# Performance work log

Measured on AMD Instinct MI355X. Metric: run time of the kernel, lower is better.

## Reference

```python
import jax, jax.numpy as jnp
import numpy as np


def setup_inputs() -> dict:
    key = jax.random.key(0)
    k1, k2 = jax.random.split(key)
    x = jax.random.normal(k1, (16, 64, 224, 224), dtype=jnp.float32)
    # conv weight [out=1, in=2, kh=7, kw=7]; init roughly mimics small-normal init
    conv_w = jax.random.normal(k2, (1, 2, 7, 7), dtype=jnp.float32) * 0.01
    conv_b = jnp.zeros((1,), dtype=jnp.float32)
    return {"x": x, "conv_w": conv_w, "conv_b": conv_b}


def reference(x, conv_w, conv_b):
    # channel-wise mean and max -> [B, 2, H, W]
    avg_out = jnp.mean(x, axis=1, keepdims=True)
    max_out = jnp.max(x, axis=1, keepdims=True)
    feat = jnp.concatenate([avg_out, max_out], axis=1)
    # 2->1 channel 7x7 conv, padding 3 (same)
    y = jax.lax.conv_general_dilated(
        feat, conv_w,
        window_strides=(1, 1),
        padding=((3, 3), (3, 3)),
        dimension_numbers=("NCHW", "OIHW", "NCHW"),
    ) + conv_b[None, :, None, None]
    # sigmoid gate broadcast-multiplied back onto x
    return jax.nn.sigmoid(y) * x
```

## Files before the change

kernel.cpp:

```cpp
#include <hip/hip_runtime.h>
#include <math.h>

#define BB 16
#define CC 64
#define HH 224
#define WW 224
#define HWSZ (HH * WW)
#define HW4 (HWSZ / 4)
#define W4 (WW / 4)
#define R 7
#define TILES (HH / R)
#define FR (R + 6)
#define FW 240
#define T 512
#define NBLK (BB * TILES)

#define TA 256
#define NPIX (BB * HW4)
#define NBLKA (NPIX / TA)

typedef float f32x4 __attribute__((ext_vector_type(4)));

__global__ __launch_bounds__(TA) void reduce_kernel(const float* __restrict__ x,
                                                    float* __restrict__ feat) {
    const int idx = blockIdx.x * TA + threadIdx.x;
    const int b   = idx / HW4;
    const int p   = idx - b * HW4;
    const f32x4* xp = reinterpret_cast<const f32x4*>(x) + (size_t)b * (CC * HW4) + p;

    f32x4 s = {0.f, 0.f, 0.f, 0.f};
    f32x4 m = {-INFINITY, -INFINITY, -INFINITY, -INFINITY};
#pragma unroll 16
    for (int c = 0; c < CC; ++c) {
        f32x4 u = xp[(size_t)c * HW4];
        s += u;
        m[0] = fmaxf(m[0], u[0]); m[1] = fmaxf(m[1], u[1]);
        m[2] = fmaxf(m[2], u[2]); m[3] = fmaxf(m[3], u[3]);
    }
    const float inv = 1.0f / 64.0f;
    f32x4* fav = reinterpret_cast<f32x4*>(feat);
    f32x4* fmx = fav + NPIX;
    fav[idx] = s * inv;
    fmx[idx] = m;
}

__global__ __launch_bounds__(T, 4) void gate_kernel(const float* __restrict__ x,
                                                    const float* __restrict__ feat,
                                                    const float* __restrict__ cw,
                                                    const float* __restrict__ cb,
                                                    float* __restrict__ out) {
    __shared__ float fa[FR * FW];
    __shared__ float fm[FR * FW];
    __shared__ alignas(16) float gate[R * WW];
    __shared__ float wt[98];

    const int blk0 = blockIdx.x;
    const int blk  = (blk0 & 7) * (NBLK / 8) + (blk0 >> 3);
    const int b    = blk >> 5;
    const int tb   = blk & 31;
    const int h0   = tb * R;
    const int t    = threadIdx.x;

    for (int i = t; i < FR * FW; i += T) { fa[i] = 0.f; fm[i] = 0.f; }
    if (t < 98) wt[t] = cw[t];
    __syncthreads();

    const f32x4* fav = reinterpret_cast<const f32x4*>(feat) + (size_t)b * HW4;
    const f32x4* fmx = fav + NPIX;
    for (int q = t; q < 2 * FR * W4; q += T) {
        int plane = (q >= FR * W4);
        int p  = plane ? q - FR * W4 : q;
        int pr = p / W4;
        int pc = p - pr * W4;
        int gh = h0 - 3 + pr;
        if ((unsigned)gh >= (unsigned)HH) continue;
        f32x4 u = (plane ? fmx : fav)[gh * W4 + pc];
        float* dst = (plane ? fm : fa) + pr * FW + 3 + pc * 4;
        dst[0] = u[0]; dst[1] = u[1]; dst[2] = u[2]; dst[3] = u[3];
    }
    __syncthreads();

    const float bias = cb[0];
    for (int p = t; p < R * WW; p += T) {
        int r = p / WW;
        int w = p - r * WW;
        float acc = bias;
#pragma unroll
        for (int kh = 0; kh < 7; ++kh) {
            int ro = (r + kh) * FW + w;
#pragma unroll
            for (int kw = 0; kw < 7; ++kw) {
                acc = fmaf(fa[ro + kw], wt[kh * 7 + kw], acc);
                acc = fmaf(fm[ro + kw], wt[49 + kh * 7 + kw], acc);
            }
        }
        gate[p] = 1.0f / (1.0f + expf(-acc));
    }
    __syncthreads();

    const f32x4* xb = reinterpret_cast<const f32x4*>(x) + (size_t)b * (CC * HW4);
    f32x4* ob = reinterpret_cast<f32x4*>(out) + (size_t)b * (CC * HW4);
    const f32x4* g4 = reinterpret_cast<const f32x4*>(gate);
    const int NP = R * W4;
    for (int i = t; i < CC * NP; i += T) {
        int c  = i / NP;
        int p  = i - c * NP;
        int pr = p / W4;
        int pc = p - pr * W4;
        size_t off = (size_t)c * HW4 + (size_t)(h0 + pr) * W4 + pc;
        f32x4 v = xb[off];
        f32x4 g = g4[p];
        v *= g;
        __builtin_nontemporal_store(v, ob + off);
    }
}

extern "C" void kernel_launch(void* const* d_in, const int* in_sizes, int n_in,
                              void* d_out, int out_size, void* d_ws, size_t ws_size,
                              hipStream_t stream) {
    const float* x  = (const float*)d_in[0];
    const float* cw = (const float*)d_in[1];
    const float* cb = (const float*)d_in[2];
    float* out  = (float*)d_out;
    float* feat = (float*)d_ws;

    reduce_kernel<<<NBLKA, TA, 0, stream>>>(x, feat);
    gate_kernel<<<NBLK, T, 0, stream>>>(x, feat, cw, cb, out);
}
```

Measured before the change: 380.4 us.

## Split fused conv-gate kernel into separate conv and elementwise multiply kernels

Breaks the fused gate kernel into a conv kernel that writes the sigmoid gate map to global workspace and a separate streaming multiply kernel. The multiply kernel loads the gate once per thread and reuses it across 16 channels with coalesced vector loads, and it runs with many more independent blocks. This is meant to raise memory-level parallelism in the dominant x read and out write pass. In exchange it adds a kernel launch and an extra global round trip for the gate map.

```diff
diff --git a/kernel.cpp b/kernel.cpp
--- a/kernel.cpp
+++ b/kernel.cpp
@@ -8,18 +8,12 @@
 #define HWSZ (HH * WW)
 #define HW4 (HWSZ / 4)
 #define W4 (WW / 4)
-#define R 7
-#define TILES (HH / R)
-#define FR (R + 6)
-#define FW 240
-#define T 512
-#define NBLK (BB * TILES)
+
+typedef float f32x4 __attribute__((ext_vector_type(4)));
 
 #define TA 256
 #define NPIX (BB * HW4)
 #define NBLKA (NPIX / TA)
-
-typedef float f32x4 __attribute__((ext_vector_type(4)));
 
 __global__ __launch_bounds__(TA) void reduce_kernel(const float* __restrict__ x,
                                                     float* __restrict__ feat) {
@@ -37,37 +31,40 @@
         m[0] = fmaxf(m[0], u[0]); m[1] = fmaxf(m[1], u[1]);
         m[2] = fmaxf(m[2], u[2]); m[3] = fmaxf(m[3], u[3]);
     }
-    const float inv = 1.0f / 64.0f;
     f32x4* fav = reinterpret_cast<f32x4*>(feat);
     f32x4* fmx = fav + NPIX;
-    fav[idx] = s * inv;
+    fav[idx] = s * (1.0f / 64.0f);
     fmx[idx] = m;
 }
 
-__global__ __launch_bounds__(T, 4) void gate_kernel(const float* __restrict__ x,
-                                                    const float* __restrict__ feat,
-                                                    const float* __restrict__ cw,
-                                                    const float* __restrict__ cb,
-                                                    float* __restrict__ out) {
+#define R 7
+#define TILES (HH / R)
+#define FR (R + 6)
+#define FW 240
+#define TC 256
+#define NBLKC (BB * TILES)
+
+__global__ __launch_bounds__(TC) void conv_kernel(const float* __restrict__ feat,
+                                                  const float* __restrict__ cw,
+                                                  const float* __restrict__ cb,
+                                                  float* __restrict__ gate) {
     __shared__ float fa[FR * FW];
     __shared__ float fm[FR * FW];
-    __shared__ alignas(16) float gate[R * WW];
     __shared__ float wt[98];
 
-    const int blk0 = blockIdx.x;
-    const int blk  = (blk0 & 7) * (NBLK / 8) + (blk0 >> 3);
-    const int b    = blk >> 5;
-    const int tb   = blk & 31;
-    const int h0   = tb * R;
-    const int t    = threadIdx.x;
+    const int blk = blockIdx.x;
+    const int b   = blk >> 5;
+    const int tb  = blk & 31;
+    const int h0  = tb * R;
+    const int t   = threadIdx.x;
 
-    for (int i = t; i < FR * FW; i += T) { fa[i] = 0.f; fm[i] = 0.f; }
+    for (int i = t; i < FR * FW; i += TC) { fa[i] = 0.f; fm[i] = 0.f; }
     if (t < 98) wt[t] = cw[t];
     __syncthreads();
 
     const f32x4* fav = reinterpret_cast<const f32x4*>(feat) + (size_t)b * HW4;
     const f32x4* fmx = fav + NPIX;
-    for (int q = t; q < 2 * FR * W4; q += T) {
+    for (int q = t; q < 2 * FR * W4; q += TC) {
         int plane = (q >= FR * W4);
         int p  = plane ? q - FR * W4 : q;
         int pr = p / W4;
@@ -81,7 +78,8 @@
     __syncthreads();
 
     const float bias = cb[0];
-    for (int p = t; p < R * WW; p += T) {
+    float* gb = gate + (size_t)b * HWSZ + (size_t)h0 * WW;
+    for (int p = t; p < R * WW; p += TC) {
         int r = p / WW;
         int w = p - r * WW;
         float acc = bias;
@@ -94,24 +92,35 @@
                 acc = fmaf(fm[ro + kw], wt[49 + kh * 7 + kw], acc);
             }
         }
-        gate[p] = 1.0f / (1.0f + expf(-acc));
+        gb[p] = 1.0f / (1.0f + expf(-acc));
     }
-    __syncthreads();
+}
 
-    const f32x4* xb = reinterpret_cast<const f32x4*>(x) + (size_t)b * (CC * HW4);
-    f32x4* ob = reinterpret_cast<f32x4*>(out) + (size_t)b * (CC * HW4);
-    const f32x4* g4 = reinterpret_cast<const f32x4*>(gate);
-    const int NP = R * W4;
-    for (int i = t; i < CC * NP; i += T) {
-        int c  = i / NP;
-        int p  = i - c * NP;
-        int pr = p / W4;
-        int pc = p - pr * W4;
-        size_t off = (size_t)c * HW4 + (size_t)(h0 + pr) * W4 + pc;
-        f32x4 v = xb[off];
-        f32x4 g = g4[p];
+#define TM 256
+#define CSPL 4
+#define CPG (CC / CSPL)
+#define CHUNKS (HW4 / TM)
+#define NBLKM (BB * CSPL * CHUNKS)
+
+__global__ __launch_bounds__(TM) void mul_kernel(const float* __restrict__ x,
+                                                 const float* __restrict__ gate,
+                                                 float* __restrict__ out) {
+    const int blk   = blockIdx.x;
+    const int chunk = blk % CHUNKS;
+    const int cg    = (blk / CHUNKS) % CSPL;
+    const int b     = blk / (CHUNKS * CSPL);
+    const int p     = chunk * TM + threadIdx.x;
+
+    const f32x4 g = reinterpret_cast<const f32x4*>(gate)[(size_t)b * HW4 + p];
+
+    const size_t base = ((size_t)b * CC + cg * CPG) * HW4 + p;
+    const f32x4* xp = reinterpret_cast<const f32x4*>(x) + base;
+    f32x4*       op = reinterpret_cast<f32x4*>(out) + base;
+#pragma unroll
+    for (int c = 0; c < CPG; ++c) {
+        f32x4 v = xp[(size_t)c * HW4];
         v *= g;
-        __builtin_nontemporal_store(v, ob + off);
+        __builtin_nontemporal_store(v, op + (size_t)c * HW4);
     }
 }
 
@@ -123,7 +132,9 @@
     const float* cb = (const float*)d_in[2];
     float* out  = (float*)d_out;
     float* feat = (float*)d_ws;
+    float* gate = feat + (size_t)2 * BB * HWSZ;
 
     reduce_kernel<<<NBLKA, TA, 0, stream>>>(x, feat);
-    gate_kernel<<<NBLK, T, 0, stream>>>(x, feat, cw, cb, out);
+    conv_kernel<<<NBLKC, TC, 0, stream>>>(feat, cw, cb, gate);
+    mul_kernel<<<NBLKM, TM, 0, stream>>>(x, gate, out);
 }
```

Result: slower. 388.3 us (+2.1%).
